# Performance work log

Hardware: AMD Instinct MI355X
Metric: run time of the kernel (lower is better)

Reference implementation:

```python
import jax, jax.numpy as jnp
import numpy as np

N_REF, N_IN, D_FEAT, P, N_ELEM = 4096, 8192, 512, 256, 4


def setup_inputs() -> dict:
    key = jax.random.key(0)
    k1, k2, k3, k4, k5 = jax.random.split(key, 5)
    return {
        "Alpha": jax.random.normal(k1, (P, N_REF), dtype=jnp.float32) * 0.05,
        "X_ref": jax.random.normal(k2, (N_REF, D_FEAT), dtype=jnp.float32),
        "desc": jax.random.normal(k3, (N_IN, D_FEAT), dtype=jnp.float32),
        "Z_ref": jax.random.randint(k4, (N_REF,), 0, N_ELEM, dtype=jnp.int32),
        "Z": jax.random.randint(k5, (N_IN,), 0, N_ELEM, dtype=jnp.int32),
        "expK": 2,
    }


def reference(Alpha, X_ref, desc, Z_ref, Z, expK):
    # Per-element grouped kernel: K[i, j] = (X_ref[i] . desc[j])**expK,
    # contribution only where ref atom i and query atom j share the element.
    # This is exactly the gather -> per-element GEMM+pow -> combine -> scatter
    # of the original module, expressed as one masked dense computation.
    K = jnp.power(jnp.matmul(X_ref, desc.T), expK)          # [N_ref, N_in]
    same_elem = Z_ref[:, None] == Z[None, :]                # [N_ref, N_in]
    K_masked = jnp.where(same_elem, K, jnp.zeros((), K.dtype))
    y = jnp.matmul(Alpha, K_masked)                          # [P, N_in]
    return y
```

## Files before the change

kernel.cpp:

```cpp
#include <hip/hip_runtime.h>
#include <stdint.h>

#define P_DIM 256
#define NREF  4096
#define NIN   8192
#define DF    512
#define NE    4
#define CREF  1536
#define CIN   2560
#define AE_LD (NE * CREF)

typedef __bf16 bf16x8 __attribute__((ext_vector_type(8)));
typedef float  f32x4  __attribute__((ext_vector_type(4)));
typedef unsigned short ush8 __attribute__((ext_vector_type(8)));

static __device__ __forceinline__ unsigned short f2bf(float f) {
    uint32_t u = __builtin_bit_cast(uint32_t, f);
    u += 0x7FFFu + ((u >> 16) & 1u);
    return (unsigned short)(u >> 16);
}

__global__ __launch_bounds__(256) void plan_sort(
    const int* __restrict__ Zr, const int* __restrict__ Z,
    int* __restrict__ iperm, int* __restrict__ jperm, int* __restrict__ cnt) {
    __shared__ int histX[NE][256];
    __shared__ int histD[NE][256];
    const int t = threadIdx.x;
    constexpr int CHX = NREF / 256;
    constexpr int CHD = NIN / 256;

    int lc[NE];
#pragma unroll
    for (int e = 0; e < NE; ++e) lc[e] = 0;
    for (int k = 0; k < CHX; ++k) lc[Zr[t * CHX + k] & (NE - 1)]++;
#pragma unroll
    for (int e = 0; e < NE; ++e) histX[e][t] = lc[e];

#pragma unroll
    for (int e = 0; e < NE; ++e) lc[e] = 0;
    for (int k = 0; k < CHD; ++k) lc[Z[t * CHD + k] & (NE - 1)]++;
#pragma unroll
    for (int e = 0; e < NE; ++e) histD[e][t] = lc[e];

    __syncthreads();
    if (t < 2 * NE) {
        int b = t & (NE - 1);
        int isD = t >> 2;
        int run = 0;
        if (!isD) {
            for (int u = 0; u < 256; ++u) { int v = histX[b][u]; histX[b][u] = run; run += v; }
            cnt[b] = run;
        } else {
            for (int u = 0; u < 256; ++u) { int v = histD[b][u]; histD[b][u] = run; run += v; }
            cnt[NE + b] = run;
        }
    }
    __syncthreads();

    int off[NE];
#pragma unroll
    for (int e = 0; e < NE; ++e) off[e] = histX[e][t];
    for (int k = 0; k < CHX; ++k) {
        int i = t * CHX + k;
        int e = Zr[i] & (NE - 1);
        iperm[e * CREF + off[e]++] = i;
    }
#pragma unroll
    for (int e = 0; e < NE; ++e) off[e] = histD[e][t];
    for (int k = 0; k < CHD; ++k) {
        int j = t * CHD + k;
        int e = Z[j] & (NE - 1);
        jperm[e * CIN + off[e]++] = j;
    }
}

__global__ void gather_pad(const float* __restrict__ X_ref, const float* __restrict__ desc,
                           const int* __restrict__ iperm, const int* __restrict__ jperm,
                           const int* __restrict__ cnt,
                           unsigned short* __restrict__ Xe, unsigned short* __restrict__ De) {
    int w = (blockIdx.x * blockDim.x + threadIdx.x) >> 6;
    int lane = threadIdx.x & 63;
    const float* src = nullptr;
    unsigned short* dstp;
    if (w < NE * CREF) {
        int e = w / CREF, s = w - e * CREF;
        if (s < cnt[e]) src = X_ref + (size_t)iperm[w] * DF;
        dstp = Xe + (size_t)w * DF;
    } else {
        int w2 = w - NE * CREF;
        int e = w2 / CIN, s = w2 - e * CIN;
        if (s < cnt[NE + e]) src = desc + (size_t)jperm[w2] * DF;
        dstp = De + (size_t)w2 * DF;
    }
    ush8 o;
    if (src) {
        float4 a = *(const float4*)(src + lane * 8);
        float4 b = *(const float4*)(src + lane * 8 + 4);
        o[0] = f2bf(a.x); o[1] = f2bf(a.y); o[2] = f2bf(a.z); o[3] = f2bf(a.w);
        o[4] = f2bf(b.x); o[5] = f2bf(b.y); o[6] = f2bf(b.z); o[7] = f2bf(b.w);
    } else {
        o = (ush8){0, 0, 0, 0, 0, 0, 0, 0};
    }
    *(ush8*)(dstp + lane * 8) = o;
}

__global__ void alpha_gather(const float* __restrict__ Alpha, const int* __restrict__ iperm,
                             const int* __restrict__ cnt, unsigned short* __restrict__ Ae) {
    int idx = blockIdx.x * blockDim.x + threadIdx.x;
    int p = idx / AE_LD;
    int col = idx - p * AE_LD;
    int e = col / CREF;
    int ic = col - e * CREF;
    unsigned short v = 0;
    if (ic < cnt[e]) v = f2bf(Alpha[(size_t)p * NREF + iperm[col]]);
    Ae[idx] = v;
}

__global__ __launch_bounds__(256) void g1_grouped(
    const unsigned short* __restrict__ DeA, const unsigned short* __restrict__ XeA,
    unsigned short* __restrict__ KtA, const int* __restrict__ cnt) {
    constexpr int BK = 64;
    const int e = blockIdx.z;
    const int padR = (cnt[e] + 127) & ~127;
    const int padI = (cnt[NE + e] + 127) & ~127;
    const int m0 = blockIdx.y * 128;
    const int n0 = blockIdx.x * 128;
    if (m0 >= padI || n0 >= padR) return;

    const unsigned short* A = DeA + (size_t)e * CIN * DF;
    const unsigned short* B = XeA + (size_t)e * CREF * DF;
    unsigned short* C = KtA + (size_t)e * CIN * CREF;

    __shared__ unsigned short tA[128 * BK];
    __shared__ unsigned short tB[128 * BK];

    const int tid = threadIdx.x, wave = tid >> 6, lane = tid & 63;
    const int wr = wave >> 1, wc = wave & 1;
    const int waveM = wr * 64, waveN = wc * 64;
    const int lrow = lane >> 3, ls = lane & 7;
    const int l15 = lane & 15, lq = lane >> 4;

    f32x4 acc[4][4];
#pragma unroll
    for (int r = 0; r < 4; ++r)
#pragma unroll
        for (int c = 0; c < 4; ++c) acc[r][c] = (f32x4){0.f, 0.f, 0.f, 0.f};

#pragma unroll 1
    for (int k0 = 0; k0 < DF; k0 += BK) {
        __syncthreads();
#pragma unroll
        for (int it = 0; it < 8; ++it) {
            int cb = wave + it * 4;
            bool isB = cb >= 16;
            int cb2 = isB ? cb - 16 : cb;
            int row = cb2 * 8 + lrow;
            int g = ls ^ (row & 7);
            const unsigned short* gp = (isB ? B : A)
                + (size_t)((isB ? n0 : m0) + row) * DF + (size_t)(k0 + g * 8);
            unsigned short* lp = (isB ? tB : tA) + cb2 * (8 * BK);
            __builtin_amdgcn_global_load_lds(
                (const __attribute__((address_space(1))) void*)gp,
                (__attribute__((address_space(3))) void*)lp, 16, 0, 0);
        }
        __syncthreads();
#pragma unroll
        for (int kk = 0; kk < BK; kk += 32) {
            const int cbase = kk >> 3;
            bf16x8 af[4], bf[4];
#pragma unroll
            for (int r = 0; r < 4; ++r) {
                int m = waveM + r * 16 + l15;
                int ch = (cbase + lq) ^ (m & 7);
                af[r] = *(const bf16x8*)&tA[m * BK + ch * 8];
            }
#pragma unroll
            for (int c = 0; c < 4; ++c) {
                int n = waveN + c * 16 + l15;
                int ch = (cbase + lq) ^ (n & 7);
                bf[c] = *(const bf16x8*)&tB[n * BK + ch * 8];
            }
#pragma unroll
            for (int r = 0; r < 4; ++r)
#pragma unroll
                for (int c = 0; c < 4; ++c)
                    acc[r][c] = __builtin_amdgcn_mfma_f32_16x16x32_bf16(
                        af[r], bf[c], acc[r][c], 0, 0, 0);
        }
    }

#pragma unroll
    for (int r = 0; r < 4; ++r) {
        int mb = m0 + waveM + r * 16 + lq * 4;
#pragma unroll
        for (int reg = 0; reg < 4; ++reg) {
            size_t ro = (size_t)(mb + reg) * CREF;
#pragma unroll
            for (int c = 0; c < 4; ++c) {
                int n = n0 + waveN + c * 16 + l15;
                float v = acc[r][c][reg];
                C[ro + n] = f2bf(v * v);
            }
        }
    }
}

__global__ __launch_bounds__(256) void g2_grouped(
    const unsigned short* __restrict__ Ae, const unsigned short* __restrict__ KtA,
    const int* __restrict__ jperm, const int* __restrict__ cnt,
    float* __restrict__ out) {
    constexpr int BK = 64;
    const int e = blockIdx.z;
    const int cntI = cnt[NE + e];
    const int padR = (cnt[e] + 127) & ~127;
    const int n0 = blockIdx.x * 64;
    const int m0 = blockIdx.y * 128;
    if (n0 >= cntI) return;

    const unsigned short* B = KtA + (size_t)e * CIN * CREF;

    __shared__ unsigned short tA[128 * BK];
    __shared__ unsigned short tB[64 * BK];

    const int tid = threadIdx.x, wave = tid >> 6, lane = tid & 63;
    const int wr = wave >> 1, wc = wave & 1;
    const int waveM = wr * 64, waveN = wc * 32;
    const int lrow = lane >> 3, ls = lane & 7;
    const int l15 = lane & 15, lq = lane >> 4;

    f32x4 acc[4][2];
#pragma unroll
    for (int r = 0; r < 4; ++r)
#pragma unroll
        for (int c = 0; c < 2; ++c) acc[r][c] = (f32x4){0.f, 0.f, 0.f, 0.f};

#pragma unroll 1
    for (int k0 = 0; k0 < padR; k0 += BK) {
        __syncthreads();
#pragma unroll
        for (int it = 0; it < 6; ++it) {
            int cb = wave + it * 4;
            bool isB = cb >= 16;
            int cb2 = isB ? cb - 16 : cb;
            int row = cb2 * 8 + lrow;
            int g = ls ^ (row & 7);
            const unsigned short* gp = isB
                ? B + (size_t)(n0 + row) * CREF + (size_t)(k0 + g * 8)
                : Ae + (size_t)(m0 + row) * AE_LD + (size_t)(e * CREF + k0 + g * 8);
            unsigned short* lp = (isB ? tB : tA) + cb2 * (8 * BK);
            __builtin_amdgcn_global_load_lds(
                (const __attribute__((address_space(1))) void*)gp,
                (__attribute__((address_space(3))) void*)lp, 16, 0, 0);
        }
        __syncthreads();
#pragma unroll
        for (int kk = 0; kk < BK; kk += 32) {
            const int cbase = kk >> 3;
            bf16x8 af[4], bf[2];
#pragma unroll
            for (int r = 0; r < 4; ++r) {
                int m = waveM + r * 16 + l15;
                int ch = (cbase + lq) ^ (m & 7);
                af[r] = *(const bf16x8*)&tA[m * BK + ch * 8];
            }
#pragma unroll
            for (int c = 0; c < 2; ++c) {
                int n = waveN + c * 16 + l15;
                int ch = (cbase + lq) ^ (n & 7);
                bf[c] = *(const bf16x8*)&tB[n * BK + ch * 8];
            }
#pragma unroll
            for (int r = 0; r < 4; ++r)
#pragma unroll
                for (int c = 0; c < 2; ++c)
                    acc[r][c] = __builtin_amdgcn_mfma_f32_16x16x32_bf16(
                        af[r], bf[c], acc[r][c], 0, 0, 0);
        }
    }

    int jok[2], jdest[2];
#pragma unroll
    for (int c = 0; c < 2; ++c) {
        int jl = n0 + waveN + c * 16 + l15;
        jok[c] = jl < cntI;
        jdest[c] = jok[c] ? jperm[e * CIN + jl] : 0;
    }
#pragma unroll
    for (int r = 0; r < 4; ++r) {
        int pb = m0 + waveM + r * 16 + lq * 4;
#pragma unroll
        for (int reg = 0; reg < 4; ++reg) {
            size_t ro = (size_t)(pb + reg) * NIN;
#pragma unroll
            for (int c = 0; c < 2; ++c)
                if (jok[c]) out[ro + jdest[c]] = acc[r][c][reg];
        }
    }
}

extern "C" void kernel_launch(void* const* d_in, const int* in_sizes, int n_in,
                              void* d_out, int out_size, void* d_ws, size_t ws_size,
                              hipStream_t stream) {
    const float* Alpha = (const float*)d_in[0];
    const float* X_ref = (const float*)d_in[1];
    const float* desc  = (const float*)d_in[2];
    const int*   Z_ref = (const int*)d_in[3];
    const int*   Z     = (const int*)d_in[4];
    float* out = (float*)d_out;

    unsigned short* Xe = (unsigned short*)d_ws;
    unsigned short* De = Xe + (size_t)NE * CREF * DF;
    unsigned short* Ae = De + (size_t)NE * CIN * DF;
    unsigned short* Kt = Ae + (size_t)P_DIM * AE_LD;
    int* iperm = (int*)(Kt + (size_t)NE * CIN * CREF);
    int* jperm = iperm + NE * CREF;
    int* cnt   = jperm + NE * CIN;

    plan_sort<<<1, 256, 0, stream>>>(Z_ref, Z, iperm, jperm, cnt);

    gather_pad<<<NE * (CREF + CIN) * 64 / 256, 256, 0, stream>>>(
        X_ref, desc, iperm, jperm, cnt, Xe, De);

    alpha_gather<<<P_DIM * AE_LD / 256, 256, 0, stream>>>(Alpha, iperm, cnt, Ae);

    g1_grouped<<<dim3(CREF / 128, CIN / 128, NE), 256, 0, stream>>>(De, Xe, Kt, cnt);

    g2_grouped<<<dim3(CIN / 64, P_DIM / 128, NE), 256, 0, stream>>>(Ae, Kt, jperm, cnt, out);
}
```

Measured before the change: 150.9 us.

## Fuse sort, gather and Alpha permute into one prep kernel; gather rows inside GEMM

Merges the single-block sort, the X/desc gather-convert and the Alpha permute into one prep launch. Each of 64 blocks recomputes the histogram and iperm in shared memory and then fills its share of the permuted Alpha, while the remaining blocks convert X_ref and desc to bf16 in their original row order, with one zero row appended to each. The first GEMM now gathers rows indirectly through iperm/jperm when issuing its direct global-to-LDS loads, which removes the padded per-element copies and two kernel launches. In exchange, the sort work is duplicated across blocks, the prep kernel uses a large amount of shared memory, and the GEMM's loads become row-indirect.

```diff
diff --git a/kernel.cpp b/kernel.cpp
--- a/kernel.cpp
+++ b/kernel.cpp
@@ -9,6 +9,7 @@
 #define CREF  1536
 #define CIN   2560
 #define AE_LD (NE * CREF)
+#define NALPHA 64
 
 typedef __bf16 bf16x8 __attribute__((ext_vector_type(8)));
 typedef float  f32x4  __attribute__((ext_vector_type(4)));
@@ -20,126 +21,146 @@
     return (unsigned short)(u >> 16);
 }
 
-__global__ __launch_bounds__(256) void plan_sort(
+__global__ __launch_bounds__(256) void prep(
+    const float* __restrict__ Alpha, const float* __restrict__ X_ref,
+    const float* __restrict__ desc,
     const int* __restrict__ Zr, const int* __restrict__ Z,
-    int* __restrict__ iperm, int* __restrict__ jperm, int* __restrict__ cnt) {
-    __shared__ int histX[NE][256];
-    __shared__ int histD[NE][256];
+    unsigned short* __restrict__ Xb, unsigned short* __restrict__ Db,
+    unsigned short* __restrict__ Ae,
+    int* __restrict__ iperm_ws, int* __restrict__ jperm_ws,
+    int* __restrict__ cnt_ws) {
+    __shared__ int hist[2 * NE * 256];
+    __shared__ int ipermL[NE * CREF];
+    __shared__ int cntS[2 * NE];
     const int t = threadIdx.x;
-    constexpr int CHX = NREF / 256;
-    constexpr int CHD = NIN / 256;
-
-    int lc[NE];
-#pragma unroll
-    for (int e = 0; e < NE; ++e) lc[e] = 0;
-    for (int k = 0; k < CHX; ++k) lc[Zr[t * CHX + k] & (NE - 1)]++;
-#pragma unroll
-    for (int e = 0; e < NE; ++e) histX[e][t] = lc[e];
-
-#pragma unroll
-    for (int e = 0; e < NE; ++e) lc[e] = 0;
-    for (int k = 0; k < CHD; ++k) lc[Z[t * CHD + k] & (NE - 1)]++;
-#pragma unroll
-    for (int e = 0; e < NE; ++e) histD[e][t] = lc[e];
-
-    __syncthreads();
-    if (t < 2 * NE) {
-        int b = t & (NE - 1);
-        int isD = t >> 2;
-        int run = 0;
-        if (!isD) {
-            for (int u = 0; u < 256; ++u) { int v = histX[b][u]; histX[b][u] = run; run += v; }
-            cnt[b] = run;
-        } else {
-            for (int u = 0; u < 256; ++u) { int v = histD[b][u]; histD[b][u] = run; run += v; }
-            cnt[NE + b] = run;
-        }
-    }
-    __syncthreads();
-
-    int off[NE];
-#pragma unroll
-    for (int e = 0; e < NE; ++e) off[e] = histX[e][t];
-    for (int k = 0; k < CHX; ++k) {
-        int i = t * CHX + k;
-        int e = Zr[i] & (NE - 1);
-        iperm[e * CREF + off[e]++] = i;
-    }
-#pragma unroll
-    for (int e = 0; e < NE; ++e) off[e] = histD[e][t];
-    for (int k = 0; k < CHD; ++k) {
-        int j = t * CHD + k;
-        int e = Z[j] & (NE - 1);
-        jperm[e * CIN + off[e]++] = j;
-    }
-}
-
-__global__ void gather_pad(const float* __restrict__ X_ref, const float* __restrict__ desc,
-                           const int* __restrict__ iperm, const int* __restrict__ jperm,
-                           const int* __restrict__ cnt,
-                           unsigned short* __restrict__ Xe, unsigned short* __restrict__ De) {
-    int w = (blockIdx.x * blockDim.x + threadIdx.x) >> 6;
-    int lane = threadIdx.x & 63;
-    const float* src = nullptr;
-    unsigned short* dstp;
-    if (w < NE * CREF) {
-        int e = w / CREF, s = w - e * CREF;
-        if (s < cnt[e]) src = X_ref + (size_t)iperm[w] * DF;
-        dstp = Xe + (size_t)w * DF;
+
+    if (blockIdx.x < NALPHA) {
+        constexpr int CHX = NREF / 256, CHD = NIN / 256;
+        int lc[NE];
+#pragma unroll
+        for (int e = 0; e < NE; ++e) lc[e] = 0;
+        for (int k = 0; k < CHX; ++k) lc[Zr[t * CHX + k] & (NE - 1)]++;
+#pragma unroll
+        for (int e = 0; e < NE; ++e) hist[e * 256 + t] = lc[e];
+#pragma unroll
+        for (int e = 0; e < NE; ++e) lc[e] = 0;
+        for (int k = 0; k < CHD; ++k) lc[Z[t * CHD + k] & (NE - 1)]++;
+#pragma unroll
+        for (int e = 0; e < NE; ++e) hist[(NE + e) * 256 + t] = lc[e];
+        __syncthreads();
+        if (t < 2 * NE) {
+            int run = 0;
+            for (int u = 0; u < 256; ++u) {
+                int v = hist[t * 256 + u]; hist[t * 256 + u] = run; run += v;
+            }
+            cntS[t] = (t < NE) ? (run > CREF ? CREF : run) : (run > CIN ? CIN : run);
+        }
+        __syncthreads();
+
+        int off[NE];
+#pragma unroll
+        for (int e = 0; e < NE; ++e) off[e] = hist[e * 256 + t];
+        for (int k = 0; k < CHX; ++k) {
+            int i = t * CHX + k;
+            int e = Zr[i] & (NE - 1);
+            int o = off[e]++;
+            if (o < CREF) ipermL[e * CREF + o] = i;
+        }
+        if (blockIdx.x == 0) {
+            int offD[NE];
+#pragma unroll
+            for (int e = 0; e < NE; ++e) offD[e] = hist[(NE + e) * 256 + t];
+            for (int k = 0; k < CHD; ++k) {
+                int j = t * CHD + k;
+                int e = Z[j] & (NE - 1);
+                int o = offD[e]++;
+                if (o < CIN) jperm_ws[e * CIN + o] = j;
+            }
+            if (t < 2 * NE) cnt_ws[t] = cntS[t];
+        }
+        __syncthreads();
+        if (blockIdx.x == 0)
+            for (int idx = t; idx < NE * CREF; idx += 256)
+                iperm_ws[idx] = ipermL[idx];
+
+        for (int idx = blockIdx.x * 256 + t; idx < P_DIM * AE_LD;
+             idx += NALPHA * 256) {
+            int p = idx / AE_LD;
+            int col = idx - p * AE_LD;
+            int e = col / CREF;
+            int ic = col - e * CREF;
+            unsigned short v = 0;
+            if (ic < cntS[e]) v = f2bf(Alpha[(size_t)p * NREF + ipermL[col]]);
+            Ae[idx] = v;
+        }
     } else {
-        int w2 = w - NE * CREF;
-        int e = w2 / CIN, s = w2 - e * CIN;
-        if (s < cnt[NE + e]) src = desc + (size_t)jperm[w2] * DF;
-        dstp = De + (size_t)w2 * DF;
-    }
-    ush8 o;
-    if (src) {
-        float4 a = *(const float4*)(src + lane * 8);
-        float4 b = *(const float4*)(src + lane * 8 + 4);
-        o[0] = f2bf(a.x); o[1] = f2bf(a.y); o[2] = f2bf(a.z); o[3] = f2bf(a.w);
-        o[4] = f2bf(b.x); o[5] = f2bf(b.y); o[6] = f2bf(b.z); o[7] = f2bf(b.w);
-    } else {
-        o = (ush8){0, 0, 0, 0, 0, 0, 0, 0};
-    }
-    *(ush8*)(dstp + lane * 8) = o;
-}
-
-__global__ void alpha_gather(const float* __restrict__ Alpha, const int* __restrict__ iperm,
-                             const int* __restrict__ cnt, unsigned short* __restrict__ Ae) {
-    int idx = blockIdx.x * blockDim.x + threadIdx.x;
-    int p = idx / AE_LD;
-    int col = idx - p * AE_LD;
-    int e = col / CREF;
-    int ic = col - e * CREF;
-    unsigned short v = 0;
-    if (ic < cnt[e]) v = f2bf(Alpha[(size_t)p * NREF + iperm[col]]);
-    Ae[idx] = v;
+        int wv = ((blockIdx.x - NALPHA) * 256 + t) >> 6;
+        int lane = t & 63;
+        int nw = (gridDim.x - NALPHA) * 4;
+        const int totalRows = (NREF + 1) + (NIN + 1);
+        for (int row = wv; row < totalRows; row += nw) {
+            const float* src;
+            unsigned short* dst;
+            if (row <= NREF) {
+                dst = Xb + (size_t)row * DF;
+                src = (row < NREF) ? X_ref + (size_t)row * DF : nullptr;
+            } else {
+                int r2 = row - (NREF + 1);
+                dst = Db + (size_t)r2 * DF;
+                src = (r2 < NIN) ? desc + (size_t)r2 * DF : nullptr;
+            }
+            ush8 o;
+            if (src) {
+                float4 a = *(const float4*)(src + lane * 8);
+                float4 b = *(const float4*)(src + lane * 8 + 4);
+                o[0] = f2bf(a.x); o[1] = f2bf(a.y); o[2] = f2bf(a.z); o[3] = f2bf(a.w);
+                o[4] = f2bf(b.x); o[5] = f2bf(b.y); o[6] = f2bf(b.z); o[7] = f2bf(b.w);
+            } else {
+                o = (ush8){0, 0, 0, 0, 0, 0, 0, 0};
+            }
+            *(ush8*)(dst + lane * 8) = o;
+        }
+    }
 }
 
 __global__ __launch_bounds__(256) void g1_grouped(
-    const unsigned short* __restrict__ DeA, const unsigned short* __restrict__ XeA,
-    unsigned short* __restrict__ KtA, const int* __restrict__ cnt) {
+    const unsigned short* __restrict__ Db, const unsigned short* __restrict__ Xb,
+    unsigned short* __restrict__ KtA,
+    const int* __restrict__ iperm, const int* __restrict__ jperm,
+    const int* __restrict__ cnt) {
     constexpr int BK = 64;
     const int e = blockIdx.z;
-    const int padR = (cnt[e] + 127) & ~127;
-    const int padI = (cnt[NE + e] + 127) & ~127;
+    const int cntR = cnt[e], cntI = cnt[NE + e];
+    const int padR = (cntR + 127) & ~127;
+    const int padI = (cntI + 127) & ~127;
     const int m0 = blockIdx.y * 128;
     const int n0 = blockIdx.x * 128;
     if (m0 >= padI || n0 >= padR) return;
 
-    const unsigned short* A = DeA + (size_t)e * CIN * DF;
-    const unsigned short* B = XeA + (size_t)e * CREF * DF;
     unsigned short* C = KtA + (size_t)e * CIN * CREF;
-
     __shared__ unsigned short tA[128 * BK];
     __shared__ unsigned short tB[128 * BK];
 
     const int tid = threadIdx.x, wave = tid >> 6, lane = tid & 63;
-    const int wr = wave >> 1, wc = wave & 1;
-    const int waveM = wr * 64, waveN = wc * 64;
+    const int waveM = (wave >> 1) * 64, waveN = (wave & 1) * 64;
     const int lrow = lane >> 3, ls = lane & 7;
     const int l15 = lane & 15, lq = lane >> 4;
 
+    const unsigned short* sb[8];
+    unsigned short* lp[8];
+#pragma unroll
+    for (int it = 0; it < 8; ++it) {
+        int cb = wave + it * 4;
+        bool isB = cb >= 16;
+        int cb2 = isB ? cb - 16 : cb;
+        int rl = cb2 * 8 + lrow;
+        int srcRow;
+        if (isB) srcRow = (n0 + rl < cntR) ? iperm[e * CREF + n0 + rl] : NREF;
+        else     srcRow = (m0 + rl < cntI) ? jperm[e * CIN + m0 + rl] : NIN;
+        sb[it] = (isB ? Xb : Db) + (size_t)srcRow * DF + (size_t)((ls ^ lrow) * 8);
+        lp[it] = (isB ? tB : tA) + cb2 * (8 * BK);
+    }
+
     f32x4 acc[4][4];
 #pragma unroll
     for (int r = 0; r < 4; ++r)
@@ -150,19 +171,10 @@
     for (int k0 = 0; k0 < DF; k0 += BK) {
         __syncthreads();
 #pragma unroll
-        for (int it = 0; it < 8; ++it) {
-            int cb = wave + it * 4;
-            bool isB = cb >= 16;
-            int cb2 = isB ? cb - 16 : cb;
-            int row = cb2 * 8 + lrow;
-            int g = ls ^ (row & 7);
-            const unsigned short* gp = (isB ? B : A)
-                + (size_t)((isB ? n0 : m0) + row) * DF + (size_t)(k0 + g * 8);
-            unsigned short* lp = (isB ? tB : tA) + cb2 * (8 * BK);
+        for (int it = 0; it < 8; ++it)
             __builtin_amdgcn_global_load_lds(
-                (const __attribute__((address_space(1))) void*)gp,
-                (__attribute__((address_space(3))) void*)lp, 16, 0, 0);
-        }
+                (const __attribute__((address_space(1))) void*)(sb[it] + k0),
+                (__attribute__((address_space(3))) void*)lp[it], 16, 0, 0);
         __syncthreads();
 #pragma unroll
         for (int kk = 0; kk < BK; kk += 32) {
@@ -218,13 +230,11 @@
     if (n0 >= cntI) return;
 
     const unsigned short* B = KtA + (size_t)e * CIN * CREF;
-
     __shared__ unsigned short tA[128 * BK];
     __shared__ unsigned short tB[64 * BK];
 
     const int tid = threadIdx.x, wave = tid >> 6, lane = tid & 63;
-    const int wr = wave >> 1, wc = wave & 1;
-    const int waveM = wr * 64, waveN = wc * 32;
+    const int waveM = (wave >> 1) * 64, waveN = (wave & 1) * 32;
     const int lrow = lane >> 3, ls = lane & 7;
     const int l15 = lane & 15, lq = lane >> 4;
 
@@ -308,22 +318,20 @@
     const int*   Z     = (const int*)d_in[4];
     float* out = (float*)d_out;
 
-    unsigned short* Xe = (unsigned short*)d_ws;
-    unsigned short* De = Xe + (size_t)NE * CREF * DF;
-    unsigned short* Ae = De + (size_t)NE * CIN * DF;
+    unsigned short* Xb = (unsigned short*)d_ws;
+    unsigned short* Db = Xb + (size_t)(NREF + 1) * DF;
+    unsigned short* Ae = Db + (size_t)(NIN + 1) * DF;
     unsigned short* Kt = Ae + (size_t)P_DIM * AE_LD;
     int* iperm = (int*)(Kt + (size_t)NE * CIN * CREF);
     int* jperm = iperm + NE * CREF;
     int* cnt   = jperm + NE * CIN;
 
-    plan_sort<<<1, 256, 0, stream>>>(Z_ref, Z, iperm, jperm, cnt);
-
-    gather_pad<<<NE * (CREF + CIN) * 64 / 256, 256, 0, stream>>>(
-        X_ref, desc, iperm, jperm, cnt, Xe, De);
-
-    alpha_gather<<<P_DIM * AE_LD / 256, 256, 0, stream>>>(Alpha, iperm, cnt, Ae);
-
-    g1_grouped<<<dim3(CREF / 128, CIN / 128, NE), 256, 0, stream>>>(De, Xe, Kt, cnt);
-
-    g2_grouped<<<dim3(CIN / 64, P_DIM / 128, NE), 256, 0, stream>>>(Ae, Kt, jperm, cnt, out);
-}
+    prep<<<512, 256, 0, stream>>>(Alpha, X_ref, desc, Z_ref, Z,
+                                  Xb, Db, Ae, iperm, jperm, cnt);
+
+    g1_grouped<<<dim3(CREF / 128, CIN / 128, NE), 256, 0, stream>>>(
+        Db, Xb, Kt, iperm, jperm, cnt);
+
+    g2_grouped<<<dim3(CIN / 64, P_DIM / 128, NE), 256, 0, stream>>>(
+        Ae, Kt, jperm, cnt, out);
+}
```

Result: slower. 180.6 us (+19.7%).

## Fuse sort, feature gather and alpha gather into one redundant-sort prep kernel

Applied to the files above, without the earlier changes.

Replaces the single-block sort kernel and the two gather kernels with one kernel. Every block recomputes the per-element histogram and permutation in shared memory, then does its share of the bf16 feature gather or the Alpha column gather. This removes two kernel launches and the serial dependency on a one-block sort. In exchange, the Z and Z_ref scans are repeated in every block, and the gather now runs on a fixed grid-stride of 512 blocks. Counts are also clamped to the padded capacities.

```diff
diff --git a/kernel.cpp b/kernel.cpp
--- a/kernel.cpp
+++ b/kernel.cpp
@@ -9,6 +9,8 @@
 #define CREF  1536
 #define CIN   2560
 #define AE_LD (NE * CREF)
+#define ROWB  416
+#define ALPB  96
 
 typedef __bf16 bf16x8 __attribute__((ext_vector_type(8)));
 typedef float  f32x4  __attribute__((ext_vector_type(4)));
@@ -20,100 +22,107 @@
     return (unsigned short)(u >> 16);
 }
 
-__global__ __launch_bounds__(256) void plan_sort(
+__global__ __launch_bounds__(256) void prep(
+    const float* __restrict__ Alpha, const float* __restrict__ X_ref,
+    const float* __restrict__ desc,
     const int* __restrict__ Zr, const int* __restrict__ Z,
-    int* __restrict__ iperm, int* __restrict__ jperm, int* __restrict__ cnt) {
-    __shared__ int histX[NE][256];
-    __shared__ int histD[NE][256];
+    unsigned short* __restrict__ Xe, unsigned short* __restrict__ De,
+    unsigned short* __restrict__ Ae,
+    int* __restrict__ jperm_ws, int* __restrict__ cnt_ws) {
+    __shared__ unsigned short ipermL[NE * CREF];
+    __shared__ unsigned short jpermL[NE * CIN];
+    __shared__ int hist[2 * NE * 256];
+    __shared__ int cntS[2 * NE];
     const int t = threadIdx.x;
-    constexpr int CHX = NREF / 256;
-    constexpr int CHD = NIN / 256;
+    constexpr int CHX = NREF / 256, CHD = NIN / 256;
 
     int lc[NE];
 #pragma unroll
     for (int e = 0; e < NE; ++e) lc[e] = 0;
     for (int k = 0; k < CHX; ++k) lc[Zr[t * CHX + k] & (NE - 1)]++;
 #pragma unroll
-    for (int e = 0; e < NE; ++e) histX[e][t] = lc[e];
-
+    for (int e = 0; e < NE; ++e) hist[e * 256 + t] = lc[e];
 #pragma unroll
     for (int e = 0; e < NE; ++e) lc[e] = 0;
     for (int k = 0; k < CHD; ++k) lc[Z[t * CHD + k] & (NE - 1)]++;
 #pragma unroll
-    for (int e = 0; e < NE; ++e) histD[e][t] = lc[e];
-
+    for (int e = 0; e < NE; ++e) hist[(NE + e) * 256 + t] = lc[e];
     __syncthreads();
     if (t < 2 * NE) {
-        int b = t & (NE - 1);
-        int isD = t >> 2;
         int run = 0;
-        if (!isD) {
-            for (int u = 0; u < 256; ++u) { int v = histX[b][u]; histX[b][u] = run; run += v; }
-            cnt[b] = run;
-        } else {
-            for (int u = 0; u < 256; ++u) { int v = histD[b][u]; histD[b][u] = run; run += v; }
-            cnt[NE + b] = run;
-        }
+        for (int u = 0; u < 256; ++u) {
+            int v = hist[t * 256 + u]; hist[t * 256 + u] = run; run += v;
+        }
+        cntS[t] = (t < NE) ? (run > CREF ? CREF : run) : (run > CIN ? CIN : run);
     }
     __syncthreads();
-
     int off[NE];
 #pragma unroll
-    for (int e = 0; e < NE; ++e) off[e] = histX[e][t];
+    for (int e = 0; e < NE; ++e) off[e] = hist[e * 256 + t];
     for (int k = 0; k < CHX; ++k) {
         int i = t * CHX + k;
         int e = Zr[i] & (NE - 1);
-        iperm[e * CREF + off[e]++] = i;
-    }
-#pragma unroll
-    for (int e = 0; e < NE; ++e) off[e] = histD[e][t];
+        int o = off[e]++;
+        if (o < CREF) ipermL[e * CREF + o] = (unsigned short)i;
+    }
+#pragma unroll
+    for (int e = 0; e < NE; ++e) off[e] = hist[(NE + e) * 256 + t];
     for (int k = 0; k < CHD; ++k) {
         int j = t * CHD + k;
         int e = Z[j] & (NE - 1);
-        jperm[e * CIN + off[e]++] = j;
-    }
-}
-
-__global__ void gather_pad(const float* __restrict__ X_ref, const float* __restrict__ desc,
-                           const int* __restrict__ iperm, const int* __restrict__ jperm,
-                           const int* __restrict__ cnt,
-                           unsigned short* __restrict__ Xe, unsigned short* __restrict__ De) {
-    int w = (blockIdx.x * blockDim.x + threadIdx.x) >> 6;
-    int lane = threadIdx.x & 63;
-    const float* src = nullptr;
-    unsigned short* dstp;
-    if (w < NE * CREF) {
-        int e = w / CREF, s = w - e * CREF;
-        if (s < cnt[e]) src = X_ref + (size_t)iperm[w] * DF;
-        dstp = Xe + (size_t)w * DF;
+        int o = off[e]++;
+        if (o < CIN) jpermL[e * CIN + o] = (unsigned short)j;
+    }
+    __syncthreads();
+
+    if (blockIdx.x == 0) {
+        for (int idx = t; idx < NE * CIN; idx += 256)
+            jperm_ws[idx] = jpermL[idx];
+        if (t < 2 * NE) cnt_ws[t] = cntS[t];
+    }
+
+    if (blockIdx.x < ROWB) {
+        int gw = (blockIdx.x * 256 + t) >> 6;
+        int lane = t & 63;
+        constexpr int NW = ROWB * 4;
+        for (int w = gw; w < NE * (CREF + CIN); w += NW) {
+            const float* src = nullptr;
+            unsigned short* dst;
+            if (w < NE * CREF) {
+                int e = w / CREF, s = w - e * CREF;
+                if (s < cntS[e]) src = X_ref + (size_t)ipermL[w] * DF;
+                dst = Xe + (size_t)w * DF;
+            } else {
+                int w2 = w - NE * CREF;
+                int e = w2 / CIN, s = w2 - e * CIN;
+                if (s < cntS[NE + e]) src = desc + (size_t)jpermL[w2] * DF;
+                dst = De + (size_t)w2 * DF;
+            }
+            ush8 o;
+            if (src) {
+                float4 a = *(const float4*)(src + lane * 8);
+                float4 b = *(const float4*)(src + lane * 8 + 4);
+                o[0] = f2bf(a.x); o[1] = f2bf(a.y); o[2] = f2bf(a.z); o[3] = f2bf(a.w);
+                o[4] = f2bf(b.x); o[5] = f2bf(b.y); o[6] = f2bf(b.z); o[7] = f2bf(b.w);
+            } else {
+                o = (ush8){0, 0, 0, 0, 0, 0, 0, 0};
+            }
+            *(ush8*)(dst + lane * 8) = o;
+        }
     } else {
-        int w2 = w - NE * CREF;
-        int e = w2 / CIN, s = w2 - e * CIN;
-        if (s < cnt[NE + e]) src = desc + (size_t)jperm[w2] * DF;
-        dstp = De + (size_t)w2 * DF;
-    }
-    ush8 o;
-    if (src) {
-        float4 a = *(const float4*)(src + lane * 8);
-        float4 b = *(const float4*)(src + lane * 8 + 4);
-        o[0] = f2bf(a.x); o[1] = f2bf(a.y); o[2] = f2bf(a.z); o[3] = f2bf(a.w);
-        o[4] = f2bf(b.x); o[5] = f2bf(b.y); o[6] = f2bf(b.z); o[7] = f2bf(b.w);
-    } else {
-        o = (ush8){0, 0, 0, 0, 0, 0, 0, 0};
-    }
-    *(ush8*)(dstp + lane * 8) = o;
-}
-
-__global__ void alpha_gather(const float* __restrict__ Alpha, const int* __restrict__ iperm,
-                             const int* __restrict__ cnt, unsigned short* __restrict__ Ae) {
-    int idx = blockIdx.x * blockDim.x + threadIdx.x;
-    int p = idx / AE_LD;
-    int col = idx - p * AE_LD;
-    int e = col / CREF;
-    int ic = col - e * CREF;
-    unsigned short v = 0;
-    if (ic < cnt[e]) v = f2bf(Alpha[(size_t)p * NREF + iperm[col]]);
-    Ae[idx] = v;
+        int b2 = blockIdx.x - ROWB;
+        int colb = b2 % (AE_LD / 256);
+        int pr = b2 / (AE_LD / 256);
+        int col = colb * 256 + t;
+        int e = col / CREF, ic = col - e * CREF;
+        int src = (ic < cntS[e]) ? (int)ipermL[col] : -1;
+        const int pend = pr * 64 + 64;
+        for (int p = pr * 64; p < pend; ++p) {
+            unsigned short v = 0;
+            if (src >= 0) v = f2bf(Alpha[(size_t)p * NREF + src]);
+            Ae[(size_t)p * AE_LD + col] = v;
+        }
+    }
 }
 
 __global__ __launch_bounds__(256) void g1_grouped(
@@ -135,8 +144,7 @@
     __shared__ unsigned short tB[128 * BK];
 
     const int tid = threadIdx.x, wave = tid >> 6, lane = tid & 63;
-    const int wr = wave >> 1, wc = wave & 1;
-    const int waveM = wr * 64, waveN = wc * 64;
+    const int waveM = (wave >> 1) * 64, waveN = (wave & 1) * 64;
     const int lrow = lane >> 3, ls = lane & 7;
     const int l15 = lane & 15, lq = lane >> 4;
 
@@ -218,13 +226,11 @@
     if (n0 >= cntI) return;
 
     const unsigned short* B = KtA + (size_t)e * CIN * CREF;
-
     __shared__ unsigned short tA[128 * BK];
     __shared__ unsigned short tB[64 * BK];
 
     const int tid = threadIdx.x, wave = tid >> 6, lane = tid & 63;
-    const int wr = wave >> 1, wc = wave & 1;
-    const int waveM = wr * 64, waveN = wc * 32;
+    const int waveM = (wave >> 1) * 64, waveN = (wave & 1) * 32;
     const int lrow = lane >> 3, ls = lane & 7;
     const int l15 = lane & 15, lq = lane >> 4;
 
@@ -312,18 +318,15 @@
     unsigned short* De = Xe + (size_t)NE * CREF * DF;
     unsigned short* Ae = De + (size_t)NE * CIN * DF;
     unsigned short* Kt = Ae + (size_t)P_DIM * AE_LD;
-    int* iperm = (int*)(Kt + (size_t)NE * CIN * CREF);
-    int* jperm = iperm + NE * CREF;
+    int* jperm = (int*)(Kt + (size_t)NE * CIN * CREF);
     int* cnt   = jperm + NE * CIN;
 
-    plan_sort<<<1, 256, 0, stream>>>(Z_ref, Z, iperm, jperm, cnt);
-
-    gather_pad<<<NE * (CREF + CIN) * 64 / 256, 256, 0, stream>>>(
-        X_ref, desc, iperm, jperm, cnt, Xe, De);
-
-    alpha_gather<<<P_DIM * AE_LD / 256, 256, 0, stream>>>(Alpha, iperm, cnt, Ae);
-
-    g1_grouped<<<dim3(CREF / 128, CIN / 128, NE), 256, 0, stream>>>(De, Xe, Kt, cnt);
-
-    g2_grouped<<<dim3(CIN / 64, P_DIM / 128, NE), 256, 0, stream>>>(Ae, Kt, jperm, cnt, out);
-}
+    prep<<<ROWB + ALPB, 256, 0, stream>>>(Alpha, X_ref, desc, Z_ref, Z,
+                                          Xe, De, Ae, jperm, cnt);
+
+    g1_grouped<<<dim3(CREF / 128, CIN / 128, NE), 256, 0, stream>>>(
+        De, Xe, Kt, cnt);
+
+    g2_grouped<<<dim3(CIN / 64, P_DIM / 128, NE), 256, 0, stream>>>(
+        Ae, Kt, jperm, cnt, out);
+}
```

New measurement: 167.9 us. 11.3% more time.
